# Optimization experiments

Hardware: AMD Instinct MI355X
Metric: run time of the kernel (lower is better)

Reference implementation:

```python
import jax, jax.numpy as jnp
import numpy as np

B, H, Q_TOK, D = 8, 12, 577, 64
N_SIDE = 24  # 24x24 = 576 patches, +1 CLS row/col -> 577


def _pairwise_dists():
    rows, cols = np.indices((N_SIDE, N_SIDE))
    idx = np.stack([rows.flatten(), cols.flatten()], axis=-1).astype(np.float32)  # (576, 2)
    d = idx[:, None, :] - idx[None, :, :]  # (576, 576, 2)
    d = np.pad(d, ((1, 0), (1, 0), (0, 0)))  # zero-pad CLS token row/col -> (577, 577, 2)
    return jnp.asarray(d)


def setup_inputs() -> dict:
    key = jax.random.key(0)
    ks = jax.random.split(key, 4)
    query = jax.random.normal(ks[0], (B, H, Q_TOK, D), jnp.float32)
    W1 = jax.random.normal(ks[1], (D, 64), jnp.float32) * 0.05
    b1 = jnp.zeros((64,), jnp.float32)
    W2 = jax.random.normal(ks[2], (64, 3), jnp.float32) * 0.05
    b2 = jnp.zeros((3,), jnp.float32)
    # uniform noise for RelaxedBernoulli reparameterized sample
    u = jax.random.uniform(ks[3], (B, H, Q_TOK, Q_TOK), jnp.float32, 1e-6, 1.0 - 1e-6)
    temperature = jnp.ones((1,), jnp.float32)
    return {"query": query, "W1": W1, "b1": b1, "W2": W2, "b2": b2,
            "dists": _pairwise_dists(), "u": u, "temperature": temperature}


def reference(query, W1, b1, W2, b2, dists, u, temperature):
    # sigma MLP: Linear -> exact GELU -> Linear, per (b,h,q) token
    hdn = jax.nn.gelu(query @ W1 + b1, approximate=False)
    sig = hdn @ W2 + b2  # (b,h,q,3)
    sy = jnp.exp(sig[..., 0]) + 1.0
    sx = jnp.exp(sig[..., 1]) + 1.0
    rho = jnp.tanh(sig[..., 2]) * 0.99
    cov = sy * sx * rho
    # 2x2 covariance matrix per query: [[sy^2, sy*sx*rho],[sy*sx*rho, sx^2]]
    Sigma = jnp.stack([jnp.stack([sy * sy, cov], -1),
                       jnp.stack([cov, sx * sx], -1)], -2)  # (b,h,q,2,2)
    # closed-form 2x2 inverse (same math as torch.linalg.inv)
    det = (sy * sx) ** 2 * (1.0 - rho * rho)
    inv00 = (sx * sx) / det
    inv11 = (sy * sy) / det
    inv01 = -cov / det
    dy = dists[..., 0]  # (q,k)
    dx = dists[..., 1]
    # Mahalanobis quadratic form, fused (no (b,h,q,k,2,2) intermediates)
    quad = (inv00[..., None] * (dy * dy)
            + 2.0 * inv01[..., None] * (dy * dx)
            + inv11[..., None] * (dx * dx))  # (b,h,q,k)
    kernel = jnp.exp(-0.5 * quad)
    probs = kernel / jnp.max(kernel, axis=-1, keepdims=True)
    probs = jnp.minimum(probs, 1.0)
    # RelaxedBernoulli rsample: sigmoid((logit(p) + logistic_noise) / T)
    logits = jnp.log(probs) - jnp.log1p(-probs)
    noise = jnp.log(u) - jnp.log1p(-u)
    mask = jax.nn.sigmoid((logits + noise) / temperature[0])
    return mask, Sigma
```

## Files before the change

kernel.cpp:

```cpp
#include <hip/hip_runtime.h>
#include <math.h>

constexpr int BB = 8, HH = 12, QT = 577, DD = 64;
constexpr int NTOK = BB * HH * QT;
constexpr long long MASK_ELEMS = (long long)NTOK * QT;
constexpr int NBH = BB * HH;
constexpr int WAVES_PER_BLOCK = 8;
constexpr int CHUNKS = NBH / WAVES_PER_BLOCK;

using f4 = __attribute__((ext_vector_type(4))) float;

template<bool T1>
__device__ __forceinline__ float mask_elem(float g0, float g1, float g2,
                                           float j0, float j1, float j2,
                                           float uv, float invT)
{
    const float hq = fmaxf(fmaf(j2, g2, fmaf(j1, g1, j0 * g0)), 0.0f);
    const float E  = __expf(hq);
    const float a  = E - 1.0f;
    if (T1)
        return __fdividef(uv, fmaf(a, 1.0f - uv, uv));
    const float rr = __fdividef(a * (1.0f - uv), uv);
    return __fdividef(1.0f, 1.0f + __expf(__logf(rr) * invT));
}

template<bool T1>
__device__ __forceinline__ void do_pass(const f4* __restrict__ G4,
                                        const int* bc, int idx, f4 uu,
                                        float* __restrict__ mp,
                                        float j0, float j1, float j2, float invT)
{
    f4 m4;
#pragma unroll
    for (int c = 0; c < 4; ++c) {
        const f4 g = G4[bc[c] + idx];
        m4[c] = mask_elem<T1>(g.x, g.y, g.z, j0, j1, j2, uu[c], invT);
    }
    __builtin_nontemporal_store(m4, (f4*)(mp + 4 * idx));
}

__global__ __launch_bounds__(512, 6)
void fused_mask(const float* __restrict__ query,
                const float* __restrict__ W1,
                const float* __restrict__ b1,
                const float* __restrict__ W2,
                const float* __restrict__ b2,
                const float* __restrict__ u,
                const float* __restrict__ temp,
                float* __restrict__ out)
{
    __shared__ f4    G4[640];
    __shared__ float W1s[DD * DD];

    f4* __restrict__ SigOut = (f4*)(out + MASK_ELEMS);
    const int q     = blockIdx.x;
    const int chunk = blockIdx.y;
    const int tid   = threadIdx.x;
    const int wave  = tid >> 6, lane = tid & 63;

    const int token = (chunk * WAVES_PER_BLOCK + wave) * QT + q;
    const unsigned base = (unsigned)token * (unsigned)QT;
    const int h  = (int)((0u - base) & 3u);
    const int NV = (QT - h) >> 2;
    const float* __restrict__ up = u   + base + h;
    float*       __restrict__ mp = out + base + h;

    const f4 uu0 = *(const f4*)(up + 4 * lane);
    const f4 uu1 = *(const f4*)(up + 4 * (64 + lane));
    const int idx2 = 128 + lane;
    f4 uu2 = {};
    if (idx2 < NV) uu2 = *(const f4*)(up + 4 * idx2);
    const int scnt = QT - 4 * NV;
    int ks = 0; float us = 0.0f;
    if (lane < scnt) {
        ks = (lane < h) ? lane : (h + 4 * NV + (lane - h));
        us = u[base + ks];
    }
    const float tval = temp[0];
    const float qv   = query[(size_t)token * DD + lane];

    ((f4*)W1s)[tid]       = ((const f4*)W1)[tid];
    ((f4*)W1s)[tid + 512] = ((const f4*)W1)[tid + 512];

    {
        const int qm1 = (q > 0) ? q - 1 : 0;
        const int qr  = (int)((unsigned)qm1 / 24u);
        const int qc  = qm1 - qr * 24;
        const float fqr = (float)qr, fqc = (float)qc;
        const bool qz = (q == 0);
        for (int k = tid; k < QT; k += 512) {
            const int km1 = (k > 0) ? k - 1 : 0;
            const int kr  = (int)((unsigned)km1 / 24u);
            const int kc  = km1 - kr * 24;
            float dy = fqr - (float)kr;
            float dx = fqc - (float)kc;
            if (qz | (k == 0)) { dy = 0.0f; dx = 0.0f; }
            f4 g; g.x = dy * dy; g.y = dy * dx; g.z = dx * dx; g.w = 0.0f;
            G4[(k & 3) * 160 + (k >> 2)] = g;
        }
    }
    __syncthreads();

    float acc = b1[lane];
#pragma unroll
    for (int i = 0; i < DD; ++i)
        acc = fmaf(__shfl(qv, i), W1s[i * DD + lane], acc);
    const float hg = 0.5f * acc * (1.0f + erff(acc * 0.7071067811865476f));

    float p0 = hg * W2[lane * 3 + 0];
    float p1 = hg * W2[lane * 3 + 1];
    float p2 = hg * W2[lane * 3 + 2];
#pragma unroll
    for (int off = 32; off > 0; off >>= 1) {
        p0 += __shfl_xor(p0, off);
        p1 += __shfl_xor(p1, off);
        p2 += __shfl_xor(p2, off);
    }
    const float sy  = expf(p0 + b2[0]) + 1.0f;
    const float sx  = expf(p1 + b2[1]) + 1.0f;
    const float rho = tanhf(p2 + b2[2]) * 0.99f;
    const float cov = sy * sx * rho;
    const float Sx = sy * sy, Sw = sx * sx, Sy = cov;
    if (lane == 0) {
        f4 s; s.x = Sx; s.y = Sy; s.z = Sy; s.w = Sw;
        SigOut[token] = s;
    }

    const float rdet = __fdividef(1.0f, fmaf(Sx, Sw, -Sy * Sy));
    const float j0 =  0.5f * Sw * rdet;
    const float j1 = -Sy * rdet;
    const float j2 =  0.5f * Sx * rdet;

    int bc[4];
#pragma unroll
    for (int c = 0; c < 4; ++c)
        bc[c] = ((h + c) & 3) * 160 + ((h + c) >> 2);

    const float invT = __int_as_float(__builtin_amdgcn_readfirstlane(
                           __float_as_int(__fdividef(1.0f, tval))));
    if (invT == 1.0f) {
        do_pass<true >(G4, bc, lane,      uu0, mp, j0, j1, j2, invT);
        do_pass<true >(G4, bc, 64 + lane, uu1, mp, j0, j1, j2, invT);
        if (idx2 < NV)
            do_pass<true >(G4, bc, idx2,  uu2, mp, j0, j1, j2, invT);
        if (lane < scnt) {
            const f4 g = G4[(ks & 3) * 160 + (ks >> 2)];
            const float m = mask_elem<true >(g.x, g.y, g.z, j0, j1, j2, us, invT);
            __builtin_nontemporal_store(m, out + base + ks);
        }
    } else {
        do_pass<false>(G4, bc, lane,      uu0, mp, j0, j1, j2, invT);
        do_pass<false>(G4, bc, 64 + lane, uu1, mp, j0, j1, j2, invT);
        if (idx2 < NV)
            do_pass<false>(G4, bc, idx2,  uu2, mp, j0, j1, j2, invT);
        if (lane < scnt) {
            const f4 g = G4[(ks & 3) * 160 + (ks >> 2)];
            const float m = mask_elem<false>(g.x, g.y, g.z, j0, j1, j2, us, invT);
            __builtin_nontemporal_store(m, out + base + ks);
        }
    }
}

extern "C" void kernel_launch(void* const* d_in, const int* in_sizes, int n_in,
                              void* d_out, int out_size, void* d_ws, size_t ws_size,
                              hipStream_t stream) {
    const float* query = (const float*)d_in[0];
    const float* W1    = (const float*)d_in[1];
    const float* b1    = (const float*)d_in[2];
    const float* W2    = (const float*)d_in[3];
    const float* b2    = (const float*)d_in[4];
    const float* u     = (const float*)d_in[6];
    const float* temp  = (const float*)d_in[7];
    float* out = (float*)d_out;

    fused_mask<<<dim3(QT, CHUNKS), dim3(512), 0, stream>>>(
        query, W1, b1, W2, b2, u, temp, out);
}
```

Measured before the change: 265.2 us.

## Drop shared memory: compute distance geometry in registers, read W1 from global

The kernel no longer stages W1 and the per-query distance table in LDS. Each lane now computes dy/dx for its keys inline with a magic-multiply divide by 24, reads W1 straight from global/L1, and uses readlane in place of shfl. Blocks shrink to 4 waves and the block-wide barrier is gone, which should raise occupancy and remove the sync and LDS traffic. In exchange there is more ALU work per element and repeated global W1 loads, though the kernel is likely bound by memory bandwidth anyway.

```diff
diff --git a/kernel.cpp b/kernel.cpp
--- a/kernel.cpp
+++ b/kernel.cpp
@@ -5,7 +5,7 @@
 constexpr int NTOK = BB * HH * QT;
 constexpr long long MASK_ELEMS = (long long)NTOK * QT;
 constexpr int NBH = BB * HH;
-constexpr int WAVES_PER_BLOCK = 8;
+constexpr int WAVES_PER_BLOCK = 4;
 constexpr int CHUNKS = NBH / WAVES_PER_BLOCK;
 
 using f4 = __attribute__((ext_vector_type(4))) float;
@@ -24,39 +24,83 @@
     return __fdividef(1.0f, 1.0f + __expf(__logf(rr) * invT));
 }
 
-template<bool T1>
-__device__ __forceinline__ void do_pass(const f4* __restrict__ G4,
-                                        const int* bc, int idx, f4 uu,
-                                        float* __restrict__ mp,
-                                        float j0, float j1, float j2, float invT)
+template<bool GUARD0>
+__device__ __forceinline__ void geom3(int kk, float fqr, float fqc, float sc,
+                                      float& g0, float& g1, float& g2)
 {
-    f4 m4;
-#pragma unroll
-    for (int c = 0; c < 4; ++c) {
-        const f4 g = G4[bc[c] + idx];
-        m4[c] = mask_elem<T1>(g.x, g.y, g.z, j0, j1, j2, uu[c], invT);
-    }
-    __builtin_nontemporal_store(m4, (f4*)(mp + 4 * idx));
+    const unsigned t  = (unsigned)(kk - 1);
+    const unsigned kr = __umulhi(t >> 3, 0xAAAAAAABu) >> 1;
+    const unsigned kc = t - kr * 24u;
+    float dy = (fqr - (float)(int)kr) * sc;
+    float dx = (fqc - (float)(int)kc) * sc;
+    if (GUARD0) { if (kk == 0) { dy = 0.0f; dx = 0.0f; } }
+    g0 = dy * dy; g1 = dy * dx; g2 = dx * dx;
 }
 
-__global__ __launch_bounds__(512, 6)
-void fused_mask(const float* __restrict__ query,
-                const float* __restrict__ W1,
-                const float* __restrict__ b1,
-                const float* __restrict__ W2,
-                const float* __restrict__ b2,
-                const float* __restrict__ u,
-                const float* __restrict__ temp,
-                float* __restrict__ out)
+template<bool T1>
+__device__ __forceinline__ void mask_row(int h, int NV, int lane,
+                                         f4 uu0, f4 uu1, f4 uu2, int idx2,
+                                         int scnt, int ks, float us,
+                                         float fqr, float fqc, float sc,
+                                         float j0, float j1, float j2,
+                                         float invT,
+                                         float* __restrict__ mp,
+                                         float* __restrict__ out, unsigned base)
 {
-    __shared__ f4    G4[640];
-    __shared__ float W1s[DD * DD];
+    const int kl = h + 4 * lane;
+    {
+        f4 m4;
+#pragma unroll
+        for (int c = 0; c < 4; ++c) {
+            float g0, g1, g2;
+            if (c == 0) geom3<true >(kl + c, fqr, fqc, sc, g0, g1, g2);
+            else        geom3<false>(kl + c, fqr, fqc, sc, g0, g1, g2);
+            m4[c] = mask_elem<T1>(g0, g1, g2, j0, j1, j2, uu0[c], invT);
+        }
+        __builtin_nontemporal_store(m4, (f4*)(mp + 4 * lane));
+    }
+    {
+        f4 m4;
+#pragma unroll
+        for (int c = 0; c < 4; ++c) {
+            float g0, g1, g2;
+            geom3<false>(kl + 256 + c, fqr, fqc, sc, g0, g1, g2);
+            m4[c] = mask_elem<T1>(g0, g1, g2, j0, j1, j2, uu1[c], invT);
+        }
+        __builtin_nontemporal_store(m4, (f4*)(mp + 4 * (64 + lane)));
+    }
+    if (idx2 < NV) {
+        f4 m4;
+#pragma unroll
+        for (int c = 0; c < 4; ++c) {
+            float g0, g1, g2;
+            geom3<false>(kl + 512 + c, fqr, fqc, sc, g0, g1, g2);
+            m4[c] = mask_elem<T1>(g0, g1, g2, j0, j1, j2, uu2[c], invT);
+        }
+        __builtin_nontemporal_store(m4, (f4*)(mp + 4 * idx2));
+    }
+    if (lane < scnt) {
+        float g0, g1, g2;
+        geom3<true>(ks, fqr, fqc, sc, g0, g1, g2);
+        const float m = mask_elem<T1>(g0, g1, g2, j0, j1, j2, us, invT);
+        __builtin_nontemporal_store(m, out + base + ks);
+    }
+}
 
+__global__ __launch_bounds__(256, 8)
+void fused_reg(const float* __restrict__ query,
+               const float* __restrict__ W1,
+               const float* __restrict__ b1,
+               const float* __restrict__ W2,
+               const float* __restrict__ b2,
+               const float* __restrict__ u,
+               const float* __restrict__ temp,
+               float* __restrict__ out)
+{
     f4* __restrict__ SigOut = (f4*)(out + MASK_ELEMS);
     const int q     = blockIdx.x;
     const int chunk = blockIdx.y;
-    const int tid   = threadIdx.x;
-    const int wave  = tid >> 6, lane = tid & 63;
+    const int wave  = threadIdx.x >> 6, lane = threadIdx.x & 63;
 
     const int token = (chunk * WAVES_PER_BLOCK + wave) * QT + q;
     const unsigned base = (unsigned)token * (unsigned)QT;
@@ -79,32 +123,14 @@
     const float tval = temp[0];
     const float qv   = query[(size_t)token * DD + lane];
 
-    ((f4*)W1s)[tid]       = ((const f4*)W1)[tid];
-    ((f4*)W1s)[tid + 512] = ((const f4*)W1)[tid + 512];
-
-    {
-        const int qm1 = (q > 0) ? q - 1 : 0;
-        const int qr  = (int)((unsigned)qm1 / 24u);
-        const int qc  = qm1 - qr * 24;
-        const float fqr = (float)qr, fqc = (float)qc;
-        const bool qz = (q == 0);
-        for (int k = tid; k < QT; k += 512) {
-            const int km1 = (k > 0) ? k - 1 : 0;
-            const int kr  = (int)((unsigned)km1 / 24u);
-            const int kc  = km1 - kr * 24;
-            float dy = fqr - (float)kr;
-            float dx = fqc - (float)kc;
-            if (qz | (k == 0)) { dy = 0.0f; dx = 0.0f; }
-            f4 g; g.x = dy * dy; g.y = dy * dx; g.z = dx * dx; g.w = 0.0f;
-            G4[(k & 3) * 160 + (k >> 2)] = g;
-        }
-    }
-    __syncthreads();
-
     float acc = b1[lane];
 #pragma unroll
-    for (int i = 0; i < DD; ++i)
-        acc = fmaf(__shfl(qv, i), W1s[i * DD + lane], acc);
+    for (int i = 0; i < DD; ++i) {
+        const float w = W1[i * DD + lane];
+        const float x = __int_as_float(
+            __builtin_amdgcn_readlane(__float_as_int(qv), i));
+        acc = fmaf(x, w, acc);
+    }
     const float hg = 0.5f * acc * (1.0f + erff(acc * 0.7071067811865476f));
 
     float p0 = hg * W2[lane * 3 + 0];
@@ -131,34 +157,20 @@
     const float j1 = -Sy * rdet;
     const float j2 =  0.5f * Sx * rdet;
 
-    int bc[4];
-#pragma unroll
-    for (int c = 0; c < 4; ++c)
-        bc[c] = ((h + c) & 3) * 160 + ((h + c) >> 2);
+    const int qm1 = (q > 0) ? q - 1 : 0;
+    const int qr  = (int)((unsigned)qm1 / 24u);
+    const int qc  = qm1 - qr * 24;
+    const float fqr = (float)qr, fqc = (float)qc;
+    const float sc  = (q == 0) ? 0.0f : 1.0f;
 
     const float invT = __int_as_float(__builtin_amdgcn_readfirstlane(
                            __float_as_int(__fdividef(1.0f, tval))));
-    if (invT == 1.0f) {
-        do_pass<true >(G4, bc, lane,      uu0, mp, j0, j1, j2, invT);
-        do_pass<true >(G4, bc, 64 + lane, uu1, mp, j0, j1, j2, invT);
-        if (idx2 < NV)
-            do_pass<true >(G4, bc, idx2,  uu2, mp, j0, j1, j2, invT);
-        if (lane < scnt) {
-            const f4 g = G4[(ks & 3) * 160 + (ks >> 2)];
-            const float m = mask_elem<true >(g.x, g.y, g.z, j0, j1, j2, us, invT);
-            __builtin_nontemporal_store(m, out + base + ks);
-        }
-    } else {
-        do_pass<false>(G4, bc, lane,      uu0, mp, j0, j1, j2, invT);
-        do_pass<false>(G4, bc, 64 + lane, uu1, mp, j0, j1, j2, invT);
-        if (idx2 < NV)
-            do_pass<false>(G4, bc, idx2,  uu2, mp, j0, j1, j2, invT);
-        if (lane < scnt) {
-            const f4 g = G4[(ks & 3) * 160 + (ks >> 2)];
-            const float m = mask_elem<false>(g.x, g.y, g.z, j0, j1, j2, us, invT);
-            __builtin_nontemporal_store(m, out + base + ks);
-        }
-    }
+    if (invT == 1.0f)
+        mask_row<true >(h, NV, lane, uu0, uu1, uu2, idx2, scnt, ks, us,
+                        fqr, fqc, sc, j0, j1, j2, invT, mp, out, base);
+    else
+        mask_row<false>(h, NV, lane, uu0, uu1, uu2, idx2, scnt, ks, us,
+                        fqr, fqc, sc, j0, j1, j2, invT, mp, out, base);
 }
 
 extern "C" void kernel_launch(void* const* d_in, const int* in_sizes, int n_in,
@@ -173,6 +185,6 @@
     const float* temp  = (const float*)d_in[7];
     float* out = (float*)d_out;
 
-    fused_mask<<<dim3(QT, CHUNKS), dim3(512), 0, stream>>>(
+    fused_reg<<<dim3(QT, CHUNKS), dim3(256), 0, stream>>>(
         query, W1, b1, W2, b2, u, temp, out);
 }
```

Measured after the change: 306.2 us. 1.15x slower.
